# Kernel optimization log

Measured on AMD Instinct MI355X. Metric: run time of the kernel, lower is better.

The kernel has to match this reference:

```python
import jax, jax.numpy as jnp
import numpy as np

EPS = 1e-12  # torch F.normalize clamp_min eps

def _l2_normalize(x):
    n = jnp.linalg.norm(x, axis=-1, keepdims=True)
    return x / jnp.maximum(n, EPS)

def setup_inputs() -> dict:
    key = jax.random.key(0)
    k1, k2 = jax.random.split(key)
    z_e = jax.random.normal(k1, (32, 256, 32, 32), dtype=jnp.float32)
    weight = jax.random.normal(k2, (1024, 256), dtype=jnp.float32)
    return {"z_e": z_e, "weight": weight}

def reference(z_e, weight):
    B, C, H, W = z_e.shape  # C == embedding_dim
    z = jnp.transpose(z_e, (0, 2, 3, 1))            # [B,H,W,C]
    flat = _l2_normalize(z.reshape(-1, C))          # [N,C]
    w_n = _l2_normalize(weight)                     # [K,C]
    # distances = 2 - 2 * <flat, w_n>; computed without grad in original
    dist = 2.0 - 2.0 * jnp.matmul(flat, w_n.T)      # [N,K]
    idx = jnp.argmin(dist, axis=1)                  # [N]
    z_q = w_n[idx].reshape(B, H, W, C)              # gather codebook rows
    z_q = jnp.transpose(z_q, (0, 3, 1, 2))          # [B,C,H,W]
    indices = idx.reshape(B, H, W)
    return z_q, indices
```

## Files before the change

### kernel.cpp

```cpp
#include <hip/hip_runtime.h>


typedef _Float16 half8 __attribute__((ext_vector_type(8)));
typedef float    floatx4 __attribute__((ext_vector_type(4)));

#define C_DIM 256
#define K_CODES 1024
#define HW 1024
#define NPIX 32768
#define NTILES 8
#define USTR 512

#define GLOAD_LDS16(g, l) __builtin_amdgcn_global_load_lds(                    \
    (const __attribute__((address_space(1))) unsigned int*)(g),                \
    (__attribute__((address_space(3))) unsigned int*)(l), 16, 0, 0)

__global__ __launch_bounds__(256) void vq_prep(
        const float* __restrict__ z, const float* __restrict__ w,
        float* __restrict__ w_n, _Float16* __restrict__ wh, _Float16* __restrict__ wl,
        _Float16* __restrict__ zh, _Float16* __restrict__ zl) {
    __shared__ float wsum[4];
    __shared__ unsigned pk[64][257];
    const int t = threadIdx.x;

    if (blockIdx.x < K_CODES) {
        const int row = blockIdx.x;
        float x = w[row * C_DIM + t];
        float s = x * x;
        #pragma unroll
        for (int off = 32; off > 0; off >>= 1) s += __shfl_down(s, off, 64);
        if ((t & 63) == 0) wsum[t >> 6] = s;
        __syncthreads();
        float tot = wsum[0] + wsum[1] + wsum[2] + wsum[3];
        float inv = 1.0f / fmaxf(sqrtf(tot), 1e-12f);
        float y = x * inv;
        w_n[row * C_DIM + t] = y;
        float ys = 16.0f * y;
        _Float16 hi = (_Float16)ys;
        wh[row * C_DIM + t] = hi;
        wl[row * C_DIM + t] = (_Float16)(ys - (float)hi);
        return;
    }

    const int zb = blockIdx.x - K_CODES;
    const int pg = zb * 64;
    const int b  = pg >> 10, p0 = pg & 1023;
    const float* zp = z + (size_t)b * C_DIM * HW + p0;

    const int cc = t >> 4, pp = (t & 15) * 4;
    #pragma unroll
    for (int it = 0; it < 16; it++) {
        const int c = it * 16 + cc;
        floatx4 v = *(const floatx4*)(zp + (size_t)c * HW + pp);
        #pragma unroll
        for (int j = 0; j < 4; j++) {
            float xs = 4.0f * v[j];
            _Float16 h = (_Float16)xs;
            _Float16 l = (_Float16)(xs - (float)h);
            pk[pp + j][c] = (unsigned)__builtin_bit_cast(unsigned short, h)
                          | ((unsigned)__builtin_bit_cast(unsigned short, l) << 16);
        }
    }
    __syncthreads();

    const int pl = t >> 4, c0 = (t & 15) * 16;
    #pragma unroll
    for (int it = 0; it < 4; it++) {
        const int p = it * 16 + pl;
        half8 hv0, hv1, lv0, lv1;
        #pragma unroll
        for (int s = 0; s < 8; s++) {
            unsigned u0 = pk[p][c0 + s];
            unsigned u1 = pk[p][c0 + 8 + s];
            hv0[s] = __builtin_bit_cast(_Float16, (unsigned short)(u0 & 0xffffu));
            lv0[s] = __builtin_bit_cast(_Float16, (unsigned short)(u0 >> 16));
            hv1[s] = __builtin_bit_cast(_Float16, (unsigned short)(u1 & 0xffffu));
            lv1[s] = __builtin_bit_cast(_Float16, (unsigned short)(u1 >> 16));
        }
        const size_t base = (size_t)(pg + p) * C_DIM + c0;
        *(half8*)(zh + base)     = hv0;
        *(half8*)(zh + base + 8) = hv1;
        *(half8*)(zl + base)     = lv0;
        *(half8*)(zl + base + 8) = lv1;
    }
}

__global__ __launch_bounds__(256, 2) void vq_gemm(
        const _Float16* __restrict__ zh, const _Float16* __restrict__ zl,
        const _Float16* __restrict__ wh, const _Float16* __restrict__ wl,
        float* __restrict__ cand_val, int* __restrict__ cand_idx) {
    __shared__ _Float16 S[2][4][8 * USTR];
    __shared__ float red_v[128][2];
    __shared__ int   red_i[128][2];

    const int tid  = threadIdx.x;
    const int lane = tid & 63, wave = tid >> 6;
    const int wm = wave >> 1, wn = wave & 1;
    const int quad = lane >> 4, l15 = lane & 15;
    const int m0 = blockIdx.x * 128, n0 = blockIdx.y * 128;

    const _Float16* ph = (wave & 2) ? wh : zh;
    const _Float16* pl_ = (wave & 2) ? wl : zl;
    const _Float16* pbase = (wave & 1) ? pl_ : ph;
    const int rbase = (wave & 2) ? n0 : m0;
    const _Float16* gsrc = pbase + (size_t)(rbase + l15) * C_DIM + quad * 8;

    floatx4 acc[4][4];
    #pragma unroll
    for (int i = 0; i < 4; i++)
        #pragma unroll
        for (int j = 0; j < 4; j++) acc[i][j] = (floatx4){0.f, 0.f, 0.f, 0.f};

    const int afrag = wm * 4, bfrag = wn * 4;

    #define STAGE(kt, nb)                                                      \
        {   const _Float16* g_ = gsrc + (kt) * 32;                             \
            _Float16* l_ = &S[(nb)][wave][0];                                  \
            _Pragma("unroll")                                                  \
            for (int u = 0; u < 8; u++)                                        \
                GLOAD_LDS16(g_ + (size_t)u * (16 * C_DIM), l_ + u * USTR);     \
        }

    STAGE(0, 0);
    int cur = 0;
    #pragma unroll
    for (int kt = 0; kt < 8; kt++) {
        __syncthreads();
        if (kt < 7) STAGE(kt + 1, cur ^ 1);

        half8 ah[4], al[4], bh[4], bl[4];
        #pragma unroll
        for (int i = 0; i < 4; i++) {
            ah[i] = *(const half8*)&S[cur][0][(afrag + i) * USTR + lane * 8];
            al[i] = *(const half8*)&S[cur][1][(afrag + i) * USTR + lane * 8];
            bh[i] = *(const half8*)&S[cur][2][(bfrag + i) * USTR + lane * 8];
            bl[i] = *(const half8*)&S[cur][3][(bfrag + i) * USTR + lane * 8];
        }
        __builtin_amdgcn_s_setprio(1);
        #pragma unroll
        for (int mi = 0; mi < 4; mi++)
            #pragma unroll
            for (int ni = 0; ni < 4; ni++) {
                acc[mi][ni] = __builtin_amdgcn_mfma_f32_16x16x32_f16(ah[mi], bh[ni], acc[mi][ni], 0, 0, 0);
                acc[mi][ni] = __builtin_amdgcn_mfma_f32_16x16x32_f16(ah[mi], bl[ni], acc[mi][ni], 0, 0, 0);
                acc[mi][ni] = __builtin_amdgcn_mfma_f32_16x16x32_f16(al[mi], bh[ni], acc[mi][ni], 0, 0, 0);
            }
        __builtin_amdgcn_s_setprio(0);
        cur ^= 1;
    }
    #undef STAGE

    #pragma unroll
    for (int mi = 0; mi < 4; mi++) {
        #pragma unroll
        for (int r = 0; r < 4; r++) {
            float bv = -__builtin_inff();
            int   bi = 0x7fffffff;
            #pragma unroll
            for (int ni = 0; ni < 4; ni++) {
                float v = acc[mi][ni][r];
                int  ci = n0 + wn * 64 + ni * 16 + l15;
                if (v > bv || (v == bv && ci < bi)) { bv = v; bi = ci; }
            }
            #pragma unroll
            for (int mk = 8; mk; mk >>= 1) {
                float ov = __shfl_xor(bv, mk, 16);
                int   oi = __shfl_xor(bi, mk, 16);
                if (ov > bv || (ov == bv && oi < bi)) { bv = ov; bi = oi; }
            }
            if (l15 == 0) {
                int row = wm * 64 + mi * 16 + quad * 4 + r;
                red_v[row][wn] = bv;
                red_i[row][wn] = bi;
            }
        }
    }
    __syncthreads();
    if (tid < 128) {
        float bv = red_v[tid][0]; int bi = red_i[tid][0];
        float v2 = red_v[tid][1]; int i2 = red_i[tid][1];
        if (v2 > bv || (v2 == bv && i2 < bi)) { bv = v2; bi = i2; }
        const int pix = m0 + tid;
        cand_val[(size_t)pix * NTILES + blockIdx.y] = bv;
        cand_idx[(size_t)pix * NTILES + blockIdx.y] = bi;
    }
}

__global__ __launch_bounds__(256) void vq_finalize(
        const float* __restrict__ cand_val,
        const int*   __restrict__ cand_idx,
        const float* __restrict__ w_n,
        float* __restrict__ zq,
        float* __restrict__ idx_out) {
    __shared__ float tile[64][257];
    __shared__ int   idx_s[64];
    const int t    = threadIdx.x;
    const int lane = t & 63, wave = t >> 6;
    const int n0   = blockIdx.x * 64;
    const int b    = n0 >> 10, p0 = n0 & 1023;

    if (t < 64) {
        const int n = n0 + t;
        const size_t base = (size_t)n * NTILES;
        float bv = cand_val[base]; int bi = cand_idx[base];
        #pragma unroll
        for (int j = 1; j < NTILES; j++) {
            float v = cand_val[base + j];
            int   c = cand_idx[base + j];
            if (v > bv || (v == bv && c < bi)) { bv = v; bi = c; }
        }
        idx_s[t] = bi;
        idx_out[n] = (float)bi;
    }
    __syncthreads();
    #pragma unroll
    for (int i = 0; i < 16; i++) {
        const int p = wave * 16 + i;
        const int row = idx_s[p];
        floatx4 v = *(const floatx4*)(w_n + (size_t)row * C_DIM + lane * 4);
        *(floatx4*)&tile[p][lane * 4] = v;
    }
    __syncthreads();
    float* zqb = zq + (size_t)b * (C_DIM * HW) + p0;
    #pragma unroll
    for (int it = 0; it < 16; it++) {
        const int c = it * 16 + wave * 4 + (lane >> 4);
        const int p = (lane & 15) * 4;
        floatx4 v = { tile[p][c], tile[p + 1][c], tile[p + 2][c], tile[p + 3][c] };
        *(floatx4*)(zqb + (size_t)c * HW + p) = v;
    }
}

extern "C" void kernel_launch(void* const* d_in, const int* in_sizes, int n_in,
                              void* d_out, int out_size, void* d_ws, size_t ws_size,
                              hipStream_t stream) {
    const float* z = (const float*)d_in[0];
    const float* w = (const float*)d_in[1];
    float* out     = (float*)d_out;

    char* ws = (char*)d_ws;
    _Float16* zh   = (_Float16*)(ws);
    _Float16* zl   = (_Float16*)(ws + (16u << 20));
    float*    w_n  = (float*)(ws + (32u << 20));
    _Float16* wh   = (_Float16*)(ws + (33u << 20));
    _Float16* wl   = (_Float16*)(ws + (33u << 20) + (1u << 19));
    float*    cval = (float*)(ws + (34u << 20));
    int*      cidx = (int*)(ws + (35u << 20));

    vq_prep<<<K_CODES + NPIX / 64, 256, 0, stream>>>(z, w, w_n, wh, wl, zh, zl);
    vq_gemm<<<dim3(NPIX / 128, NTILES), 256, 0, stream>>>(zh, zl, wh, wl, cval, cidx);
    vq_finalize<<<NPIX / 64, 256, 0, stream>>>(cval, cidx, w_n, out, out + 8388608);
}
```

Before: 194.1 us.

## Single-buffer GEMM LDS and raise occupancy to five blocks per CU

Replaces the double-buffered LDS staging in vq_gemm with one buffer that is loaded and synchronized inside every k-step, and reuses that buffer for the argmax reduction scratch. Launch bounds go from 2 to 5 blocks per CU, and the s_setprio hints and full k-loop unroll are removed. The goal is to hide global-to-LDS latency through more resident blocks rather than software prefetch. The cost is an extra barrier per k-step with no overlap inside a block, plus tighter register limits that could cause spills with a 64-float accumulator.

```diff
diff --git a/kernel.cpp b/kernel.cpp
--- a/kernel.cpp
+++ b/kernel.cpp
@@ -85,13 +85,13 @@
     }
 }
 
-__global__ __launch_bounds__(256, 2) void vq_gemm(
+__global__ __launch_bounds__(256, 5) void vq_gemm(
         const _Float16* __restrict__ zh, const _Float16* __restrict__ zl,
         const _Float16* __restrict__ wh, const _Float16* __restrict__ wl,
         float* __restrict__ cand_val, int* __restrict__ cand_idx) {
-    __shared__ _Float16 S[2][4][8 * USTR];
-    __shared__ float red_v[128][2];
-    __shared__ int   red_i[128][2];
+    __shared__ _Float16 S[4][8 * USTR];
+    float* red_v = (float*)&S[0][0];
+    int*   red_i = (int*)&S[0][1024];
 
     const int tid  = threadIdx.x;
     const int lane = tid & 63, wave = tid >> 6;
@@ -99,7 +99,7 @@
     const int quad = lane >> 4, l15 = lane & 15;
     const int m0 = blockIdx.x * 128, n0 = blockIdx.y * 128;
 
-    const _Float16* ph = (wave & 2) ? wh : zh;
+    const _Float16* ph  = (wave & 2) ? wh : zh;
     const _Float16* pl_ = (wave & 2) ? wl : zl;
     const _Float16* pbase = (wave & 1) ? pl_ : ph;
     const int rbase = (wave & 2) ? n0 : m0;
@@ -113,30 +113,24 @@
 
     const int afrag = wm * 4, bfrag = wn * 4;
 
-    #define STAGE(kt, nb)                                                      \
-        {   const _Float16* g_ = gsrc + (kt) * 32;                             \
-            _Float16* l_ = &S[(nb)][wave][0];                                  \
-            _Pragma("unroll")                                                  \
-            for (int u = 0; u < 8; u++)                                        \
-                GLOAD_LDS16(g_ + (size_t)u * (16 * C_DIM), l_ + u * USTR);     \
-        }
-
-    STAGE(0, 0);
-    int cur = 0;
-    #pragma unroll
     for (int kt = 0; kt < 8; kt++) {
         __syncthreads();
-        if (kt < 7) STAGE(kt + 1, cur ^ 1);
+        {   const _Float16* g_ = gsrc + kt * 32;
+            _Float16* l_ = &S[wave][0];
+            #pragma unroll
+            for (int u = 0; u < 8; u++)
+                GLOAD_LDS16(g_ + (size_t)u * (16 * C_DIM), l_ + u * USTR);
+        }
+        __syncthreads();
 
         half8 ah[4], al[4], bh[4], bl[4];
         #pragma unroll
         for (int i = 0; i < 4; i++) {
-            ah[i] = *(const half8*)&S[cur][0][(afrag + i) * USTR + lane * 8];
-            al[i] = *(const half8*)&S[cur][1][(afrag + i) * USTR + lane * 8];
-            bh[i] = *(const half8*)&S[cur][2][(bfrag + i) * USTR + lane * 8];
-            bl[i] = *(const half8*)&S[cur][3][(bfrag + i) * USTR + lane * 8];
-        }
-        __builtin_amdgcn_s_setprio(1);
+            ah[i] = *(const half8*)&S[0][(afrag + i) * USTR + lane * 8];
+            al[i] = *(const half8*)&S[1][(afrag + i) * USTR + lane * 8];
+            bh[i] = *(const half8*)&S[2][(bfrag + i) * USTR + lane * 8];
+            bl[i] = *(const half8*)&S[3][(bfrag + i) * USTR + lane * 8];
+        }
         #pragma unroll
         for (int mi = 0; mi < 4; mi++)
             #pragma unroll
@@ -145,10 +139,9 @@
                 acc[mi][ni] = __builtin_amdgcn_mfma_f32_16x16x32_f16(ah[mi], bl[ni], acc[mi][ni], 0, 0, 0);
                 acc[mi][ni] = __builtin_amdgcn_mfma_f32_16x16x32_f16(al[mi], bh[ni], acc[mi][ni], 0, 0, 0);
             }
-        __builtin_amdgcn_s_setprio(0);
-        cur ^= 1;
-    }
-    #undef STAGE
+    }
+
+    __syncthreads();
 
     #pragma unroll
     for (int mi = 0; mi < 4; mi++) {
@@ -170,15 +163,15 @@
             }
             if (l15 == 0) {
                 int row = wm * 64 + mi * 16 + quad * 4 + r;
-                red_v[row][wn] = bv;
-                red_i[row][wn] = bi;
+                red_v[row * 2 + wn] = bv;
+                red_i[row * 2 + wn] = bi;
             }
         }
     }
     __syncthreads();
     if (tid < 128) {
-        float bv = red_v[tid][0]; int bi = red_i[tid][0];
-        float v2 = red_v[tid][1]; int i2 = red_i[tid][1];
+        float bv = red_v[tid * 2 + 0]; int bi = red_i[tid * 2 + 0];
+        float v2 = red_v[tid * 2 + 1]; int i2 = red_i[tid * 2 + 1];
         if (v2 > bv || (v2 == bv && i2 < bi)) { bv = v2; bi = i2; }
         const int pix = m0 + tid;
         cand_val[(size_t)pix * NTILES + blockIdx.y] = bv;
```

New measurement: 276.8 us. 1.43x slower.

## Pre-swizzle operands into MFMA fragment layout and load directly to registers

Applied to the files above, without the earlier changes.

The prep kernel now writes z and codebook hi/lo halves in a fragment-major layout matching the MFMA 16x16x32 operand order. The GEMM then drops its LDS staging and barriers and loads fragments straight from global memory into registers, double-buffered across k-steps. This removes LDS traffic and block-wide syncs but doubles global/L2 reads, since the two waves sharing an A or B tile each fetch it separately. It also raises register pressure under launch_bounds(256,2).

```diff
diff --git a/kernel.cpp b/kernel.cpp
--- a/kernel.cpp
+++ b/kernel.cpp
@@ -9,23 +9,18 @@
 #define HW 1024
 #define NPIX 32768
 #define NTILES 8
-#define USTR 512
-
-#define GLOAD_LDS16(g, l) __builtin_amdgcn_global_load_lds(                    \
-    (const __attribute__((address_space(1))) unsigned int*)(g),                \
-    (__attribute__((address_space(3))) unsigned int*)(l), 16, 0, 0)
 
 __global__ __launch_bounds__(256) void vq_prep(
         const float* __restrict__ z, const float* __restrict__ w,
-        float* __restrict__ w_n, _Float16* __restrict__ wh, _Float16* __restrict__ wl,
-        _Float16* __restrict__ zh, _Float16* __restrict__ zl) {
+        float* __restrict__ w_n, _Float16* __restrict__ wfh, _Float16* __restrict__ wfl,
+        _Float16* __restrict__ zfh, _Float16* __restrict__ zfl) {
     __shared__ float wsum[4];
     __shared__ unsigned pk[64][257];
     const int t = threadIdx.x;
 
     if (blockIdx.x < K_CODES) {
-        const int row = blockIdx.x;
-        float x = w[row * C_DIM + t];
+        const int c = blockIdx.x;
+        float x = w[c * C_DIM + t];
         float s = x * x;
         #pragma unroll
         for (int off = 32; off > 0; off >>= 1) s += __shfl_down(s, off, 64);
@@ -34,11 +29,15 @@
         float tot = wsum[0] + wsum[1] + wsum[2] + wsum[3];
         float inv = 1.0f / fmaxf(sqrtf(tot), 1e-12f);
         float y = x * inv;
-        w_n[row * C_DIM + t] = y;
+        w_n[c * C_DIM + t] = y;
         float ys = 16.0f * y;
         _Float16 hi = (_Float16)ys;
-        wh[row * C_DIM + t] = hi;
-        wl[row * C_DIM + t] = (_Float16)(ys - (float)hi);
+        _Float16 lo = (_Float16)(ys - (float)hi);
+        const int kt = t >> 5, l = ((t >> 3) & 3) * 16 + (c & 15), j = t & 7;
+        const size_t fo = ((size_t)(c >> 6) * 8 + kt) * 2048 + ((c >> 4) & 3) * 512
+                        + l * 8 + j;
+        wfh[fo] = hi;
+        wfl[fo] = lo;
         return;
     }
 
@@ -63,33 +62,27 @@
     }
     __syncthreads();
 
-    const int pl = t >> 4, c0 = (t & 15) * 16;
-    #pragma unroll
-    for (int it = 0; it < 4; it++) {
-        const int p = it * 16 + pl;
-        half8 hv0, hv1, lv0, lv1;
-        #pragma unroll
-        for (int s = 0; s < 8; s++) {
-            unsigned u0 = pk[p][c0 + s];
-            unsigned u1 = pk[p][c0 + 8 + s];
-            hv0[s] = __builtin_bit_cast(_Float16, (unsigned short)(u0 & 0xffffu));
-            lv0[s] = __builtin_bit_cast(_Float16, (unsigned short)(u0 >> 16));
-            hv1[s] = __builtin_bit_cast(_Float16, (unsigned short)(u1 & 0xffffu));
-            lv1[s] = __builtin_bit_cast(_Float16, (unsigned short)(u1 >> 16));
-        }
-        const size_t base = (size_t)(pg + p) * C_DIM + c0;
-        *(half8*)(zh + base)     = hv0;
-        *(half8*)(zh + base + 8) = hv1;
-        *(half8*)(zl + base)     = lv0;
-        *(half8*)(zl + base + 8) = lv1;
+    const int u = t >> 6, l = t & 63;
+    const int row = u * 16 + (l & 15);
+    #pragma unroll
+    for (int kt = 0; kt < 8; kt++) {
+        half8 hv, lv;
+        #pragma unroll
+        for (int j = 0; j < 8; j++) {
+            unsigned v = pk[row][kt * 32 + (l >> 4) * 8 + j];
+            hv[j] = __builtin_bit_cast(_Float16, (unsigned short)(v & 0xffffu));
+            lv[j] = __builtin_bit_cast(_Float16, (unsigned short)(v >> 16));
+        }
+        const size_t fo = ((size_t)zb * 8 + kt) * 2048 + u * 512 + l * 8;
+        *(half8*)(zfh + fo) = hv;
+        *(half8*)(zfl + fo) = lv;
     }
 }
 
 __global__ __launch_bounds__(256, 2) void vq_gemm(
-        const _Float16* __restrict__ zh, const _Float16* __restrict__ zl,
-        const _Float16* __restrict__ wh, const _Float16* __restrict__ wl,
+        const _Float16* __restrict__ zfh, const _Float16* __restrict__ zfl,
+        const _Float16* __restrict__ wfh, const _Float16* __restrict__ wfl,
         float* __restrict__ cand_val, int* __restrict__ cand_idx) {
-    __shared__ _Float16 S[2][4][8 * USTR];
     __shared__ float red_v[128][2];
     __shared__ int   red_i[128][2];
 
@@ -99,11 +92,12 @@
     const int quad = lane >> 4, l15 = lane & 15;
     const int m0 = blockIdx.x * 128, n0 = blockIdx.y * 128;
 
-    const _Float16* ph = (wave & 2) ? wh : zh;
-    const _Float16* pl_ = (wave & 2) ? wl : zl;
-    const _Float16* pbase = (wave & 1) ? pl_ : ph;
-    const int rbase = (wave & 2) ? n0 : m0;
-    const _Float16* gsrc = pbase + (size_t)(rbase + l15) * C_DIM + quad * 8;
+    const size_t aoff = (size_t)(blockIdx.x * 2 + wm) * 8 * 2048 + lane * 8;
+    const size_t boff = (size_t)(blockIdx.y * 2 + wn) * 8 * 2048 + lane * 8;
+    const _Float16* pAh = zfh + aoff;
+    const _Float16* pAl = zfl + aoff;
+    const _Float16* pBh = wfh + boff;
+    const _Float16* pBl = wfl + boff;
 
     floatx4 acc[4][4];
     #pragma unroll
@@ -111,44 +105,44 @@
         #pragma unroll
         for (int j = 0; j < 4; j++) acc[i][j] = (floatx4){0.f, 0.f, 0.f, 0.f};
 
-    const int afrag = wm * 4, bfrag = wn * 4;
-
-    #define STAGE(kt, nb)                                                      \
-        {   const _Float16* g_ = gsrc + (kt) * 32;                             \
-            _Float16* l_ = &S[(nb)][wave][0];                                  \
+    half8 A0h[4], A0l[4], B0h[4], B0l[4];
+    half8 A1h[4], A1l[4], B1h[4], B1l[4];
+
+#define LOADK(AH, AL, BH, BL, kt)                                              \
+    {   _Pragma("unroll")                                                      \
+        for (int i = 0; i < 4; i++) {                                          \
+            AH[i] = *(const half8*)(pAh + (kt) * 2048 + i * 512);              \
+            AL[i] = *(const half8*)(pAl + (kt) * 2048 + i * 512);              \
+            BH[i] = *(const half8*)(pBh + (kt) * 2048 + i * 512);              \
+            BL[i] = *(const half8*)(pBl + (kt) * 2048 + i * 512);              \
+        }                                                                      \
+    }
+
+#define MFMAK(AH, AL, BH, BL)                                                  \
+    {   _Pragma("unroll")                                                      \
+        for (int mi = 0; mi < 4; mi++)                                         \
             _Pragma("unroll")                                                  \
-            for (int u = 0; u < 8; u++)                                        \
-                GLOAD_LDS16(g_ + (size_t)u * (16 * C_DIM), l_ + u * USTR);     \
-        }
-
-    STAGE(0, 0);
-    int cur = 0;
-    #pragma unroll
-    for (int kt = 0; kt < 8; kt++) {
-        __syncthreads();
-        if (kt < 7) STAGE(kt + 1, cur ^ 1);
-
-        half8 ah[4], al[4], bh[4], bl[4];
-        #pragma unroll
-        for (int i = 0; i < 4; i++) {
-            ah[i] = *(const half8*)&S[cur][0][(afrag + i) * USTR + lane * 8];
-            al[i] = *(const half8*)&S[cur][1][(afrag + i) * USTR + lane * 8];
-            bh[i] = *(const half8*)&S[cur][2][(bfrag + i) * USTR + lane * 8];
-            bl[i] = *(const half8*)&S[cur][3][(bfrag + i) * USTR + lane * 8];
-        }
-        __builtin_amdgcn_s_setprio(1);
-        #pragma unroll
-        for (int mi = 0; mi < 4; mi++)
-            #pragma unroll
-            for (int ni = 0; ni < 4; ni++) {
-                acc[mi][ni] = __builtin_amdgcn_mfma_f32_16x16x32_f16(ah[mi], bh[ni], acc[mi][ni], 0, 0, 0);
-                acc[mi][ni] = __builtin_amdgcn_mfma_f32_16x16x32_f16(ah[mi], bl[ni], acc[mi][ni], 0, 0, 0);
-                acc[mi][ni] = __builtin_amdgcn_mfma_f32_16x16x32_f16(al[mi], bh[ni], acc[mi][ni], 0, 0, 0);
-            }
-        __builtin_amdgcn_s_setprio(0);
-        cur ^= 1;
-    }
-    #undef STAGE
+            for (int ni = 0; ni < 4; ni++) {                                   \
+                acc[mi][ni] = __builtin_amdgcn_mfma_f32_16x16x32_f16(          \
+                    AH[mi], BH[ni], acc[mi][ni], 0, 0, 0);                     \
+                acc[mi][ni] = __builtin_amdgcn_mfma_f32_16x16x32_f16(          \
+                    AH[mi], BL[ni], acc[mi][ni], 0, 0, 0);                     \
+                acc[mi][ni] = __builtin_amdgcn_mfma_f32_16x16x32_f16(          \
+                    AL[mi], BH[ni], acc[mi][ni], 0, 0, 0);                     \
+            }                                                                  \
+    }
+
+    LOADK(A0h, A0l, B0h, B0l, 0);
+    LOADK(A1h, A1l, B1h, B1l, 1);  MFMAK(A0h, A0l, B0h, B0l);
+    LOADK(A0h, A0l, B0h, B0l, 2);  MFMAK(A1h, A1l, B1h, B1l);
+    LOADK(A1h, A1l, B1h, B1l, 3);  MFMAK(A0h, A0l, B0h, B0l);
+    LOADK(A0h, A0l, B0h, B0l, 4);  MFMAK(A1h, A1l, B1h, B1l);
+    LOADK(A1h, A1l, B1h, B1l, 5);  MFMAK(A0h, A0l, B0h, B0l);
+    LOADK(A0h, A0l, B0h, B0l, 6);  MFMAK(A1h, A1l, B1h, B1l);
+    LOADK(A1h, A1l, B1h, B1l, 7);  MFMAK(A0h, A0l, B0h, B0l);
+                                   MFMAK(A1h, A1l, B1h, B1l);
+#undef LOADK
+#undef MFMAK
 
     #pragma unroll
     for (int mi = 0; mi < 4; mi++) {
@@ -239,15 +233,15 @@
     float* out     = (float*)d_out;
 
     char* ws = (char*)d_ws;
-    _Float16* zh   = (_Float16*)(ws);
-    _Float16* zl   = (_Float16*)(ws + (16u << 20));
+    _Float16* zfh  = (_Float16*)(ws);
+    _Float16* zfl  = (_Float16*)(ws + (16u << 20));
     float*    w_n  = (float*)(ws + (32u << 20));
-    _Float16* wh   = (_Float16*)(ws + (33u << 20));
-    _Float16* wl   = (_Float16*)(ws + (33u << 20) + (1u << 19));
+    _Float16* wfh  = (_Float16*)(ws + (33u << 20));
+    _Float16* wfl  = (_Float16*)(ws + (33u << 20) + (1u << 19));
     float*    cval = (float*)(ws + (34u << 20));
     int*      cidx = (int*)(ws + (35u << 20));
 
-    vq_prep<<<K_CODES + NPIX / 64, 256, 0, stream>>>(z, w, w_n, wh, wl, zh, zl);
-    vq_gemm<<<dim3(NPIX / 128, NTILES), 256, 0, stream>>>(zh, zl, wh, wl, cval, cidx);
+    vq_prep<<<K_CODES + NPIX / 64, 256, 0, stream>>>(z, w, w_n, wfh, wfl, zfh, zfl);
+    vq_gemm<<<dim3(NPIX / 128, NTILES), 256, 0, stream>>>(zfh, zfl, wfh, wfl, cval, cidx);
     vq_finalize<<<NPIX / 64, 256, 0, stream>>>(cval, cidx, w_n, out, out + 8388608);
 }
```

New measurement: 161.1 us. -17.0%, faster.
